# Performance work log

Hardware: AMD Instinct MI355X
Metric: run time of the kernel (lower is better)

The kernel has to match this reference:

```python
import jax, jax.numpy as jnp
import numpy as np

B, L, P = 64, 256, 32
LANE_DIM, EMBED, DEPTH, HEADS = 2, 128, 4, 8
MLP = 4 * EMBED
HD = EMBED // HEADS
MASK_RATIO, ELIG = 0.5, 5


def _glorot(key, shape):
    lim = float(np.sqrt(6.0 / (shape[-2] + shape[-1])))
    return jax.random.uniform(key, shape, jnp.float32, -lim, lim)


def setup_inputs() -> dict:
    key = jax.random.key(0)
    ks = jax.random.split(key, 24)
    lane_positions = jax.random.normal(ks[0], (B, L, P, LANE_DIM), jnp.float32)
    lane_centers = jax.random.normal(ks[1], (B, L, LANE_DIM), jnp.float32)
    lane_angles = jax.random.normal(ks[2], (B, L), jnp.float32)
    # ragged padding + random masking, precomputed (externalizes torch randperm loop)
    rng = np.random.default_rng(0)
    pad = rng.random((B, L, P)) < 0.2  # True = padding
    valid = ~pad
    num_valid = valid.sum(-1)                      # (B,L)
    eligible = num_valid > ELIG
    num_mask = (num_valid * MASK_RATIO).astype(np.int32)  # trunc == .int()
    scores = np.where(valid, rng.random((B, L, P)), 2.0)
    rank = scores.argsort(-1).argsort(-1)          # rank of each valid point
    sel = (rank < num_mask[..., None]) & valid & eligible[..., None]
    inp = {
        'lane_positions': lane_positions,
        'lane_centers': lane_centers,
        'lane_angles': lane_angles,
        'lane_padding_mask': jnp.asarray(pad),
        'sel_mask': jnp.asarray(sel),
        'Wp': _glorot(ks[3], (LANE_DIM, EMBED)), 'bp': jnp.zeros((EMBED,)),
        'Wpe1': _glorot(ks[4], (4, EMBED)), 'bpe1': jnp.zeros((EMBED,)),
        'Wpe2': _glorot(ks[5], (EMBED, EMBED)), 'bpe2': jnp.zeros((EMBED,)),
        'lane_type': 0.02 * jax.random.normal(ks[6], (EMBED,), jnp.float32),
        'mask_token': 0.02 * jax.random.normal(ks[7], (EMBED,), jnp.float32),
        'Wqkv': _glorot(ks[8], (DEPTH, EMBED, 3 * EMBED)), 'bqkv': jnp.zeros((DEPTH, 3 * EMBED)),
        'Wo': _glorot(ks[9], (DEPTH, EMBED, EMBED)), 'bo': jnp.zeros((DEPTH, EMBED)),
        'ln1_s': jnp.ones((DEPTH, EMBED)), 'ln1_b': jnp.zeros((DEPTH, EMBED)),
        'Wm1': _glorot(ks[10], (DEPTH, EMBED, MLP)), 'bm1': jnp.zeros((DEPTH, MLP)),
        'Wm2': _glorot(ks[11], (DEPTH, MLP, EMBED)), 'bm2': jnp.zeros((DEPTH, EMBED)),
        'ln2_s': jnp.ones((DEPTH, EMBED)), 'ln2_b': jnp.zeros((DEPTH, EMBED)),
        'lnf_s': jnp.ones((EMBED,)), 'lnf_b': jnp.zeros((EMBED,)),
        'Wd1': _glorot(ks[12], (EMBED, MLP)), 'bd1': jnp.zeros((MLP,)),
        'Wd2': _glorot(ks[13], (MLP, LANE_DIM)), 'bd2': jnp.zeros((LANE_DIM,)),
    }
    return inp


def _ln(x, s, b):
    m = jnp.mean(x, -1, keepdims=True)
    v = jnp.var(x, -1, keepdims=True)
    return (x - m) * jax.lax.rsqrt(v + 1e-5) * s + b


def _forward(lane_positions, lane_centers, lane_angles, Wp, bp, Wpe1, bpe1,
             Wpe2, bpe2, lane_type, mask_token, Wqkv, bqkv, Wo, bo, ln1_s,
             ln1_b, Wm1, bm1, Wm2, bm2, ln2_s, ln2_b, lnf_s, lnf_b, Wd1, bd1,
             Wd2, bd2, sel_mask):
    lane_norm = lane_positions - lane_centers[:, :, None, :]      # (B,L,P,2)
    feat = lane_norm @ Wp + bp                                    # (B,L,P,E)
    pos_feat = jnp.concatenate([lane_centers,
                                jnp.cos(lane_angles)[..., None],
                                jnp.sin(lane_angles)[..., None]], -1)  # (B,L,4)
    pe = jax.nn.gelu(pos_feat @ Wpe1 + bpe1, approximate=False) @ Wpe2 + bpe2
    tok = feat + pe[:, :, None, :] + lane_type
    tok = jnp.where(sel_mask[..., None], mask_token, tok)
    x = tok.reshape(B * L, P, EMBED)
    scale = 1.0 / np.sqrt(HD).astype(np.float32)
    for i in range(DEPTH):  # SpaNet: pre-LN transformer encoder over points
        h = _ln(x, ln1_s[i], ln1_b[i])
        q, k, v = jnp.split(h @ Wqkv[i] + bqkv[i], 3, axis=-1)
        q = q.reshape(B * L, P, HEADS, HD)
        k = k.reshape(B * L, P, HEADS, HD)
        v = v.reshape(B * L, P, HEADS, HD)
        att = jax.nn.softmax(jnp.einsum('nqhd,nkhd->nhqk', q, k) * scale, -1)
        o = jnp.einsum('nhqk,nkhd->nqhd', att, v).reshape(B * L, P, EMBED)
        x = x + o @ Wo[i] + bo[i]
        h = _ln(x, ln2_s[i], ln2_b[i])
        x = x + jax.nn.gelu(h @ Wm1[i] + bm1[i], approximate=False) @ Wm2[i] + bm2[i]
    x = _ln(x, lnf_s, lnf_b)
    y = (jax.nn.relu(x @ Wd1 + bd1) @ Wd2 + bd2).reshape(B, L, P, LANE_DIM)
    selc = sel_mask[..., None].astype(y.dtype)
    sq = (y - lane_norm) ** 2
    loss = jnp.sum(sq * selc) / jnp.maximum(jnp.sum(selc) * LANE_DIM, 1.0)
    return loss, y


def reference(lane_positions, lane_centers, lane_angles, lane_padding_mask,
              sel_mask, Wp, bp, Wpe1, bpe1, Wpe2, bpe2, lane_type, mask_token,
              Wqkv, bqkv, Wo, bo, ln1_s, ln1_b, Wm1, bm1, Wm2, bm2, ln2_s,
              ln2_b, lnf_s, lnf_b, Wd1, bd1, Wd2, bd2):
    del lane_padding_mask  # already folded into sel_mask during setup
    return _forward(lane_positions, lane_centers, lane_angles, Wp, bp, Wpe1,
                    bpe1, Wpe2, bpe2, lane_type, mask_token, Wqkv, bqkv, Wo,
                    bo, ln1_s, ln1_b, Wm1, bm1, Wm2, bm2, ln2_s, ln2_b, lnf_s,
                    lnf_b, Wd1, bd1, Wd2, bd2, sel_mask)
```

## Files before the change

kernel.cpp:

```cpp
#include <hip/hip_runtime.h>


#define NP 32
#define NE 128
#define NSEQ (64 * 256)
#define NMLP 512
#define NDEPTH 4
#define LST 132
#define HBS 136
#define H1C 264
#define QS  24
#define PS  40
#define VST 40

#define QKV_W_OFF 0
#define O_W_OFF   196608
#define M1_W_OFF  262144
#define M2_W_OFF  524288
#define D1_W_OFF  786432
#define W_TOTAL   851968

typedef unsigned short u16;
typedef unsigned int u32;
typedef __attribute__((ext_vector_type(8))) short bf16x8;
typedef __attribute__((ext_vector_type(4))) float f32x4;
typedef __attribute__((ext_vector_type(16))) float f32x16;
#define MFMA16 __builtin_amdgcn_mfma_f32_16x16x32_bf16
#define MFMA32 __builtin_amdgcn_mfma_f32_32x32x16_bf16

__device__ __forceinline__ float b2f(u16 u) {
  union { u32 i; float f; } v; v.i = ((u32)u) << 16; return v.f;
}
__device__ __forceinline__ u16 f2b(float f) {
  union { float f; u32 i; } v; v.f = f;
  u32 x = v.i;
  x += 0x7fffu + ((x >> 16) & 1u);
  return (u16)(x >> 16);
}
__device__ __forceinline__ u32 pk2(float lo, float hi) {
  return (u32)f2b(lo) | ((u32)f2b(hi) << 16);
}

__device__ __forceinline__ float gelu_f(float x) {
  float u = x * x;
  float a2 = x * fmaf(u, 0.07135481627466029f, 1.5957691216057308f);
  float e = __expf(a2);
  float r = __builtin_amdgcn_rcpf(e + 1.0f);
  return fmaf(-x, r, x);
}

struct Args {
  const float *pos, *ctr, *ang;
  const int *sel;
  const float *Wp, *bp, *Wpe1, *bpe1, *Wpe2, *bpe2, *ltype, *mtok;
  const float *Wqkv, *bqkv, *Wo, *bo, *ln1s, *ln1b, *Wm1, *bm1, *Wm2, *bm2;
  const float *ln2s, *ln2b, *lnfs, *lnfb, *Wd1, *bd1, *Wd2, *bd2;
  float* out;
  float* wsf;
  int* wsi;
};

__global__ void pack_w(const float* __restrict__ src, u16* __restrict__ dst,
                       int K, int N, int L, int scaleN, float scale) {
  int id = blockIdx.x * 256 + threadIdx.x;
  int KT = K >> 5, NT = N >> 4;
  int total = L * NT * KT * 64;
  if (id >= total) return;
  int lane = id & 63;
  int rest = id >> 6;
  int kt = rest % KT;
  int rest2 = rest / KT;
  int nt = rest2 % NT;
  int l = rest2 / NT;
  int col = nt * 16 + (lane & 15);
  float sc = (col < scaleN) ? scale : 1.0f;
  const float* s = src + (size_t)l * K * N + (size_t)(kt * 32 + (lane >> 4) * 8) * N + col;
  u16 tmp[8];
#pragma unroll
  for (int j = 0; j < 8; ++j) tmp[j] = f2b(s[(size_t)j * N] * sc);
  ((uint4*)dst)[id] = *(const uint4*)tmp;
}

template <int NTW>
__device__ __forceinline__ void gemm_kt4_b(const u16* __restrict__ hA,
                                           const u16* __restrict__ B, int w,
                                           int lane, const float* __restrict__ bias,
                                           f32x4 (&acc)[NTW][2]) {
  int ar = lane & 15, ac = (lane >> 4) * 8;
  bf16x8 af[8];
#pragma unroll
  for (int kb = 0; kb < 4; ++kb) {
    af[kb]     = *(const bf16x8*)(hA + ar * HBS + kb * 32 + ac);
    af[kb + 4] = *(const bf16x8*)(hA + (ar + 16) * HBS + kb * 32 + ac);
  }
#pragma unroll
  for (int i = 0; i < NTW; ++i) {
    int nt = w + 4 * i;
    const u16* Bp = B + (size_t)nt * 2048 + lane * 8;
    float bb = bias[nt * 16 + ar];
    f32x4 bi = {bb, bb, bb, bb};
    acc[i][0] = bi; acc[i][1] = bi;
#pragma unroll
    for (int kb = 0; kb < 4; ++kb) {
      bf16x8 b = *(const bf16x8*)(Bp + kb * 512);
      acc[i][0] = MFMA16(af[kb], b, acc[i][0], 0, 0, 0);
      acc[i][1] = MFMA16(af[kb + 4], b, acc[i][1], 0, 0, 0);
    }
  }
}

__device__ __forceinline__ void gemm_kt8_acc(const u16* __restrict__ hA,
                                             const u16* __restrict__ B, int ktoff,
                                             int w, int lane, f32x4 (&acc)[2][2]) {
  int ar = lane & 15, ac = (lane >> 4) * 8;
#pragma unroll
  for (int ktl = 0; ktl < 8; ++ktl) {
    bf16x8 a0 = *(const bf16x8*)(hA + ar * H1C + ktl * 32 + ac);
    bf16x8 a1 = *(const bf16x8*)(hA + (ar + 16) * H1C + ktl * 32 + ac);
#pragma unroll
    for (int i = 0; i < 2; ++i) {
      int nt = w + 4 * i;
      bf16x8 b = *(const bf16x8*)(B + (size_t)nt * 8192 + (size_t)(ktoff + ktl) * 512 + lane * 8);
      acc[i][0] = MFMA16(a0, b, acc[i][0], 0, 0, 0);
      acc[i][1] = MFMA16(a1, b, acc[i][1], 0, 0, 0);
    }
  }
}

__device__ __forceinline__ void layer_norm_bf(const float* __restrict__ src,
                                              u16* __restrict__ dst,
                                              const float* gam, const float* bet,
                                              int t, float* mrow, float* vrow) {
  int p = t >> 3, j0 = (t & 7) * 16;
  const float* row = src + p * LST + j0;
  float sum = 0.f, sq = 0.f;
#pragma unroll
  for (int k = 0; k < 16; ++k) { float v = row[k]; sum += v; sq += v * v; }
#pragma unroll
  for (int o = 1; o < 8; o <<= 1) { sum += __shfl_xor(sum, o); sq += __shfl_xor(sq, o); }
  if ((t & 7) == 0) {
    float m = sum * 0.0078125f;
    mrow[p] = m;
    vrow[p] = sq * 0.0078125f - m * m;
  }
  __syncthreads();
  float m = mrow[p], rs = rsqrtf(vrow[p] + 1e-5f);
  u32 wb[8];
#pragma unroll
  for (int k8 = 0; k8 < 4; ++k8) {
    float4 v = ((const float4*)row)[k8];
    float4 g = ((const float4*)(gam + j0))[k8];
    float4 b = ((const float4*)(bet + j0))[k8];
    wb[k8 * 2]     = pk2(fmaf((v.x - m) * rs, g.x, b.x), fmaf((v.y - m) * rs, g.y, b.y));
    wb[k8 * 2 + 1] = pk2(fmaf((v.z - m) * rs, g.z, b.z), fmaf((v.w - m) * rs, g.w, b.w));
  }
  uint4* dp = (uint4*)(dst + p * HBS + j0);
  dp[0] = make_uint4(wb[0], wb[1], wb[2], wb[3]);
  dp[1] = make_uint4(wb[4], wb[5], wb[6], wb[7]);
  __syncthreads();
}

__global__ __launch_bounds__(256, 3) void mrm_main_mfma(Args a, const u16* __restrict__ wsW) {
  __shared__ float xs[32 * LST];
  __shared__ __align__(16) u16 hbf[32 * HBS];
  __shared__ __align__(16) u16 uniu[10496];
  __shared__ float mrow[32], vrow[32];
  __shared__ int selv[32];
  __shared__ float lacc;

  u16* h1c = uniu;
  float* wd2s = (float*)(uniu + 8448);
  float* tvec = (float*)uniu;
  float* pvec = (float*)uniu + 128;

  const int s = blockIdx.x;
  const int t = threadIdx.x;
  const int w = t >> 6, lane = t & 63;
  const int cr = lane & 15, rq = (lane >> 4) * 4;
  const int rg = t >> 5, cg = t & 31, r0 = rg * 4, c0 = cg * 4;
  const int l15 = lane & 15, gl = lane >> 4;
  const int l31 = lane & 31, hi5 = lane >> 5;

  if (t == 0) lacc = 0.f;
  if (t < 32) selv[t] = a.sel[s * NP + t];

  const float cx = a.ctr[s * 2 + 0];
  const float cy = a.ctr[s * 2 + 1];
  const float an = a.ang[s];
  const float ca = __cosf(an), sa = __sinf(an);

  if (t < 128) {
    float accp = a.bpe1[t] + cx * a.Wpe1[t] + cy * a.Wpe1[128 + t]
               + ca * a.Wpe1[256 + t] + sa * a.Wpe1[384 + t];
    tvec[t] = gelu_f(accp);
  }
  __syncthreads();
  if (t < 128) {
    float accp = a.bpe2[t];
    for (int e = 0; e < 128; ++e) accp += tvec[e] * a.Wpe2[e * 128 + t];
    pvec[t] = accp;
  }
  __syncthreads();

  {
    float4 w0v = *(const float4*)(a.Wp + c0);
    float4 w1v = *(const float4*)(a.Wp + NE + c0);
    float4 bpv = *(const float4*)(a.bp + c0);
    float4 ltv = *(const float4*)(a.ltype + c0);
    float4 mtv = *(const float4*)(a.mtok + c0);
    float a0 = bpv.x + pvec[c0 + 0] + ltv.x;
    float a1 = bpv.y + pvec[c0 + 1] + ltv.y;
    float a2 = bpv.z + pvec[c0 + 2] + ltv.z;
    float a3 = bpv.w + pvec[c0 + 3] + ltv.w;
#pragma unroll
    for (int rr = 0; rr < 4; ++rr) {
      int p = r0 + rr;
      float px = a.pos[(s * NP + p) * 2 + 0] - cx;
      float py = a.pos[(s * NP + p) * 2 + 1] - cy;
      bool mk = selv[p] != 0;
      float4 o;
      o.x = mk ? mtv.x : (px * w0v.x + py * w1v.x + a0);
      o.y = mk ? mtv.y : (px * w0v.y + py * w1v.y + a1);
      o.z = mk ? mtv.z : (px * w0v.z + py * w1v.z + a2);
      o.w = mk ? mtv.w : (px * w0v.w + py * w1v.w + a3);
      *(float4*)&xs[p * LST + c0] = o;
    }
  }
  __syncthreads();

  u16* qb2 = uniu + w * 768;
  u16* kb2 = uniu + 3072 + w * 768;
  u16* vb2 = uniu + 6144 + w * 640;

  for (int li = 0; li < NDEPTH; ++li) {
    const u16* qkvW = wsW + QKV_W_OFF + li * 49152;
    const u16* oW   = wsW + O_W_OFF   + li * 16384;
    const u16* m1W  = wsW + M1_W_OFF  + li * 65536;
    const u16* m2W  = wsW + M2_W_OFF  + li * 65536;
    const float* bqkv_i = a.bqkv + li * 384;
    const float* bo_i   = a.bo + li * NE;
    const float* bm1_i  = a.bm1 + li * NMLP;
    const float* bm2_i  = a.bm2 + li * NE;

    layer_norm_bf(xs, hbf, a.ln1s + li * NE, a.ln1b + li * NE, t, mrow, vrow);

    u32 opk[2][2][2];
#pragma unroll
    for (int p = 0; p < 2; ++p) {
      const int hh = 4 * p + w;
      f32x4 acc[3][2];
      {
        int ar = lane & 15, ac = (lane >> 4) * 8;
        bf16x8 af[8];
#pragma unroll
        for (int kb = 0; kb < 4; ++kb) {
          af[kb]     = *(const bf16x8*)(hbf + ar * HBS + kb * 32 + ac);
          af[kb + 4] = *(const bf16x8*)(hbf + (ar + 16) * HBS + kb * 32 + ac);
        }
#pragma unroll
        for (int i = 0; i < 3; ++i) {
          int nt = i * 8 + hh;
          const u16* Bp = qkvW + (size_t)nt * 2048 + lane * 8;
          float bb = bqkv_i[nt * 16 + ar];
          if (i == 0) bb *= 0.25f;
          f32x4 bi = {bb, bb, bb, bb};
          acc[i][0] = bi; acc[i][1] = bi;
#pragma unroll
          for (int kb = 0; kb < 4; ++kb) {
            bf16x8 b = *(const bf16x8*)(Bp + kb * 512);
            acc[i][0] = MFMA16(af[kb], b, acc[i][0], 0, 0, 0);
            acc[i][1] = MFMA16(af[kb + 4], b, acc[i][1], 0, 0, 0);
          }
        }
      }
      {
#pragma unroll
        for (int j = 0; j < 4; ++j) {
          qb2[(rq + j) * QS + cr]      = f2b(acc[0][0][j]);
          qb2[(rq + j + 16) * QS + cr] = f2b(acc[0][1][j]);
          kb2[(rq + j) * QS + cr]      = f2b(acc[1][0][j]);
          kb2[(rq + j + 16) * QS + cr] = f2b(acc[1][1][j]);
        }
        u32* vbw = (u32*)vb2 + cr * 20 + (rq >> 1);
        vbw[0] = pk2(acc[2][0][0], acc[2][0][1]);
        vbw[1] = pk2(acc[2][0][2], acc[2][0][3]);
        vbw[8] = pk2(acc[2][1][0], acc[2][1][1]);
        vbw[9] = pk2(acc[2][1][2], acc[2][1][3]);
      }
      {
        bf16x8 kf = *(const bf16x8*)(kb2 + l31 * QS + hi5 * 8);
        bf16x8 qf = *(const bf16x8*)(qb2 + l31 * QS + hi5 * 8);
        f32x16 z16 = {0.f,0.f,0.f,0.f,0.f,0.f,0.f,0.f,0.f,0.f,0.f,0.f,0.f,0.f,0.f,0.f};
        f32x16 S = MFMA32(kf, qf, z16, 0, 0, 0);
        float mx = S[0];
#pragma unroll
        for (int r = 1; r < 16; ++r) mx = fmaxf(mx, S[r]);
        mx = fmaxf(mx, __shfl_xor(mx, 32));
        float sum = 0.f;
#pragma unroll
        for (int r = 0; r < 16; ++r) { S[r] = __expf(S[r] - mx); sum += S[r]; }
        sum += __shfl_xor(sum, 32);
        float inv = __builtin_amdgcn_rcpf(sum);
        u16* pb = ((l31 < 16) ? qb2 : kb2) + (l31 & 15) * PS;
#pragma unroll
        for (int i2 = 0; i2 < 8; ++i2) {
          int key0 = ((2 * i2) & 3) + 8 * (i2 >> 1) + 4 * hi5;
          *(u32*)(pb + key0) = pk2(S[2 * i2] * inv, S[2 * i2 + 1] * inv);
        }
        bf16x8 vf = *(const bf16x8*)(vb2 + l15 * VST + gl * 8);
        const f32x4 z = {0.f, 0.f, 0.f, 0.f};
#pragma unroll
        for (int qt = 0; qt < 2; ++qt) {
          bf16x8 pa = *(const bf16x8*)(((qt == 0) ? qb2 : kb2) + l15 * PS + gl * 8);
          f32x4 o = MFMA16(pa, vf, z, 0, 0, 0);
          opk[p][qt][0] = pk2(o[0], o[1]);
          opk[p][qt][1] = pk2(o[2], o[3]);
        }
      }
    }
    __syncthreads();
#pragma unroll
    for (int p = 0; p < 2; ++p) {
      const int hh = 4 * p + w;
#pragma unroll
      for (int qt = 0; qt < 2; ++qt) {
        u16* dst = hbf + (qt * 16 + gl * 4) * HBS + hh * 16 + l15;
        dst[0 * HBS] = (u16)opk[p][qt][0];
        dst[1 * HBS] = (u16)(opk[p][qt][0] >> 16);
        dst[2 * HBS] = (u16)opk[p][qt][1];
        dst[3 * HBS] = (u16)(opk[p][qt][1] >> 16);
      }
    }
    __syncthreads();

    {
      f32x4 acc[2][2];
      gemm_kt4_b<2>(hbf, oW, w, lane, bo_i, acc);
#pragma unroll
      for (int i = 0; i < 2; ++i) {
        int n = (w + 4 * i) * 16 + cr;
#pragma unroll
        for (int j = 0; j < 4; ++j) {
          xs[(rq + j) * LST + n]      += acc[i][0][j];
          xs[(rq + j + 16) * LST + n] += acc[i][1][j];
        }
      }
    }
    __syncthreads();

    layer_norm_bf(xs, hbf, a.ln2s + li * NE, a.ln2b + li * NE, t, mrow, vrow);

    {
      f32x4 acc2[2][2];
#pragma unroll
      for (int i = 0; i < 2; ++i) {
        float bb = bm2_i[(w + 4 * i) * 16 + cr];
        f32x4 bi = {bb, bb, bb, bb};
        acc2[i][0] = bi; acc2[i][1] = bi;
      }
#pragma unroll
      for (int ch = 0; ch < 2; ++ch) {
        {
          f32x4 acc[4][2];
          gemm_kt4_b<4>(hbf, m1W + ch * 32768, w, lane, bm1_i + ch * 256, acc);
#pragma unroll
          for (int i = 0; i < 4; ++i) {
            int nl = (w + 4 * i) * 16 + cr;
#pragma unroll
            for (int j = 0; j < 4; ++j) {
              h1c[(rq + j) * H1C + nl]      = f2b(gelu_f(acc[i][0][j]));
              h1c[(rq + j + 16) * H1C + nl] = f2b(gelu_f(acc[i][1][j]));
            }
          }
        }
        __syncthreads();
        gemm_kt8_acc(h1c, m2W, ch * 8, w, lane, acc2);
        __syncthreads();
      }
#pragma unroll
      for (int i = 0; i < 2; ++i) {
        int n = (w + 4 * i) * 16 + cr;
#pragma unroll
        for (int j = 0; j < 4; ++j) {
          xs[(rq + j) * LST + n]      += acc2[i][0][j];
          xs[(rq + j + 16) * LST + n] += acc2[i][1][j];
        }
      }
    }
    __syncthreads();
  }

  layer_norm_bf(xs, hbf, a.lnfs, a.lnfb, t, mrow, vrow);

  for (int i = t; i < 1024; i += 256) wd2s[i] = a.Wd2[i];

  float yacc = 0.f;
  const int pdec = t >> 3, dd2 = (t >> 2) & 1, q4 = t & 3;
#pragma unroll
  for (int ch = 0; ch < 2; ++ch) {
    {
      f32x4 acc[4][2];
      gemm_kt4_b<4>(hbf, wsW + D1_W_OFF + ch * 32768, w, lane, a.bd1 + ch * 256, acc);
#pragma unroll
      for (int i = 0; i < 4; ++i) {
        int nl = (w + 4 * i) * 16 + cr;
#pragma unroll
        for (int j = 0; j < 4; ++j) {
          h1c[(rq + j) * H1C + nl]      = f2b(fmaxf(acc[i][0][j], 0.f));
          h1c[(rq + j + 16) * H1C + nl] = f2b(fmaxf(acc[i][1][j], 0.f));
        }
      }
    }
    __syncthreads();
    {
      const u16* hrow = h1c + pdec * H1C + q4 * 64;
      const float* wp = wd2s + (ch * 256 + q4 * 64) * 2 + dd2;
#pragma unroll
      for (int k8 = 0; k8 < 8; ++k8) {
        bf16x8 hv = *(const bf16x8*)(hrow + k8 * 8);
#pragma unroll
        for (int jj = 0; jj < 8; ++jj)
          yacc += b2f((u16)hv[jj]) * wp[(k8 * 8 + jj) * 2];
      }
    }
    __syncthreads();
  }

  {
    yacc += __shfl_xor(yacc, 1);
    yacc += __shfl_xor(yacc, 2);
    if (q4 == 0) {
      float y = yacc + a.bd2[dd2];
      a.out[1 + (s * NP + pdec) * 2 + dd2] = y;
      float lnm = a.pos[(s * NP + pdec) * 2 + dd2] - (dd2 ? cy : cx);
      float d = y - lnm;
      if (selv[pdec] != 0) atomicAdd(&lacc, d * d);
    }
  }
  __syncthreads();
  if (t == 0) {
    atomicAdd(a.wsf, lacc);
    int cnt = 0;
#pragma unroll
    for (int p = 0; p < NP; ++p) cnt += (selv[p] != 0) ? 1 : 0;
    atomicAdd(a.wsi, cnt);
  }
}

__global__ void mrm_fin(const float* ws, float* out) {
  float num = ws[0];
  int cnt = ((const int*)ws)[1];
  float den = fmaxf((float)cnt * 2.0f, 1.0f);
  out[0] = num / den;
}

extern "C" void kernel_launch(void* const* d_in, const int* in_sizes, int n_in,
                              void* d_out, int out_size, void* d_ws, size_t ws_size,
                              hipStream_t stream) {
  (void)in_sizes; (void)n_in; (void)out_size; (void)ws_size;
  Args a;
  a.pos   = (const float*)d_in[0];
  a.ctr   = (const float*)d_in[1];
  a.ang   = (const float*)d_in[2];
  a.sel   = (const int*)d_in[4];
  a.Wp    = (const float*)d_in[5];
  a.bp    = (const float*)d_in[6];
  a.Wpe1  = (const float*)d_in[7];
  a.bpe1  = (const float*)d_in[8];
  a.Wpe2  = (const float*)d_in[9];
  a.bpe2  = (const float*)d_in[10];
  a.ltype = (const float*)d_in[11];
  a.mtok  = (const float*)d_in[12];
  a.Wqkv  = (const float*)d_in[13];
  a.bqkv  = (const float*)d_in[14];
  a.Wo    = (const float*)d_in[15];
  a.bo    = (const float*)d_in[16];
  a.ln1s  = (const float*)d_in[17];
  a.ln1b  = (const float*)d_in[18];
  a.Wm1   = (const float*)d_in[19];
  a.bm1   = (const float*)d_in[20];
  a.Wm2   = (const float*)d_in[21];
  a.bm2   = (const float*)d_in[22];
  a.ln2s  = (const float*)d_in[23];
  a.ln2b  = (const float*)d_in[24];
  a.lnfs  = (const float*)d_in[25];
  a.lnfb  = (const float*)d_in[26];
  a.Wd1   = (const float*)d_in[27];
  a.bd1   = (const float*)d_in[28];
  a.Wd2   = (const float*)d_in[29];
  a.bd2   = (const float*)d_in[30];
  a.out   = (float*)d_out;
  a.wsf   = (float*)d_ws;
  a.wsi   = ((int*)d_ws) + 1;

  hipMemsetAsync(d_ws, 0, 8, stream);
  u16* wsW = (u16*)((char*)d_ws + 64);
  pack_w<<<dim3(96),  dim3(256), 0, stream>>>(a.Wqkv, wsW + QKV_W_OFF, 128, 384, 4, 128, 0.25f);
  pack_w<<<dim3(32),  dim3(256), 0, stream>>>(a.Wo,   wsW + O_W_OFF,   128, 128, 4, 0, 1.f);
  pack_w<<<dim3(128), dim3(256), 0, stream>>>(a.Wm1,  wsW + M1_W_OFF,  128, 512, 4, 0, 1.f);
  pack_w<<<dim3(128), dim3(256), 0, stream>>>(a.Wm2,  wsW + M2_W_OFF,  512, 128, 4, 0, 1.f);
  pack_w<<<dim3(32),  dim3(256), 0, stream>>>(a.Wd1,  wsW + D1_W_OFF,  128, 512, 1, 0, 1.f);
  mrm_main_mfma<<<dim3(NSEQ), dim3(256), 0, stream>>>(a, wsW);
  mrm_fin<<<dim3(1), dim3(1), 0, stream>>>((const float*)d_ws, (float*)d_out);
}
```

Measured before the change: 2.131 ms.

## Keep residual stream in registers, shrink LDS, raise occupancy to four blocks

The fp32 residual tile moves from shared memory into per-thread registers laid out to match the MFMA output fragments. Layer norm becomes a register-based macro that reduces partial sums through a small shared buffer. The Wd2 shared copy is dropped, its reads now come from global memory, and positions are staged once in shared memory. With the smaller LDS footprint, launch bounds rise from three to four blocks per CU. Other changes: bf16 conversion now uses the library intrinsic, and the softmax max/sum use tree reductions. The risks are higher register pressure under the tighter bound and an extra barrier in each layer norm.

```diff
diff --git a/kernel.cpp b/kernel.cpp
--- a/kernel.cpp
+++ b/kernel.cpp
@@ -1,4 +1,5 @@
 #include <hip/hip_runtime.h>
+#include <hip/hip_bf16.h>
 
 
 #define NP 32
@@ -6,12 +7,12 @@
 #define NSEQ (64 * 256)
 #define NMLP 512
 #define NDEPTH 4
-#define LST 132
 #define HBS 136
 #define H1C 264
 #define QS  24
 #define PS  40
 #define VST 40
+#define PBS 66
 
 #define QKV_W_OFF 0
 #define O_W_OFF   196608
@@ -32,10 +33,8 @@
   union { u32 i; float f; } v; v.i = ((u32)u) << 16; return v.f;
 }
 __device__ __forceinline__ u16 f2b(float f) {
-  union { float f; u32 i; } v; v.f = f;
-  u32 x = v.i;
-  x += 0x7fffu + ((x >> 16) & 1u);
-  return (u16)(x >> 16);
+  __hip_bfloat16 h = __float2bfloat16(f);
+  union { __hip_bfloat16 h; u16 u; } v; v.h = h; return v.u;
 }
 __device__ __forceinline__ u32 pk2(float lo, float hi) {
   return (u32)f2b(lo) | ((u32)f2b(hi) << 16);
@@ -127,49 +126,17 @@
   }
 }
 
-__device__ __forceinline__ void layer_norm_bf(const float* __restrict__ src,
-                                              u16* __restrict__ dst,
-                                              const float* gam, const float* bet,
-                                              int t, float* mrow, float* vrow) {
-  int p = t >> 3, j0 = (t & 7) * 16;
-  const float* row = src + p * LST + j0;
-  float sum = 0.f, sq = 0.f;
-#pragma unroll
-  for (int k = 0; k < 16; ++k) { float v = row[k]; sum += v; sq += v * v; }
-#pragma unroll
-  for (int o = 1; o < 8; o <<= 1) { sum += __shfl_xor(sum, o); sq += __shfl_xor(sq, o); }
-  if ((t & 7) == 0) {
-    float m = sum * 0.0078125f;
-    mrow[p] = m;
-    vrow[p] = sq * 0.0078125f - m * m;
-  }
-  __syncthreads();
-  float m = mrow[p], rs = rsqrtf(vrow[p] + 1e-5f);
-  u32 wb[8];
-#pragma unroll
-  for (int k8 = 0; k8 < 4; ++k8) {
-    float4 v = ((const float4*)row)[k8];
-    float4 g = ((const float4*)(gam + j0))[k8];
-    float4 b = ((const float4*)(bet + j0))[k8];
-    wb[k8 * 2]     = pk2(fmaf((v.x - m) * rs, g.x, b.x), fmaf((v.y - m) * rs, g.y, b.y));
-    wb[k8 * 2 + 1] = pk2(fmaf((v.z - m) * rs, g.z, b.z), fmaf((v.w - m) * rs, g.w, b.w));
-  }
-  uint4* dp = (uint4*)(dst + p * HBS + j0);
-  dp[0] = make_uint4(wb[0], wb[1], wb[2], wb[3]);
-  dp[1] = make_uint4(wb[4], wb[5], wb[6], wb[7]);
-  __syncthreads();
-}
-
-__global__ __launch_bounds__(256, 3) void mrm_main_mfma(Args a, const u16* __restrict__ wsW) {
-  __shared__ float xs[32 * LST];
+__global__ __launch_bounds__(256, 4) void mrm_main_mfma(Args a, const u16* __restrict__ wsW) {
   __shared__ __align__(16) u16 hbf[32 * HBS];
-  __shared__ __align__(16) u16 uniu[10496];
+  __shared__ __align__(16) u16 uniu[8704];
+  __shared__ float posb[64];
   __shared__ float mrow[32], vrow[32];
   __shared__ int selv[32];
   __shared__ float lacc;
 
   u16* h1c = uniu;
-  float* wd2s = (float*)(uniu + 8448);
+  float* pbufS = (float*)uniu;
+  float* pbufQ = (float*)(uniu + 4224);
   float* tvec = (float*)uniu;
   float* pvec = (float*)uniu + 128;
 
@@ -177,12 +144,12 @@
   const int t = threadIdx.x;
   const int w = t >> 6, lane = t & 63;
   const int cr = lane & 15, rq = (lane >> 4) * 4;
-  const int rg = t >> 5, cg = t & 31, r0 = rg * 4, c0 = cg * 4;
   const int l15 = lane & 15, gl = lane >> 4;
   const int l31 = lane & 31, hi5 = lane >> 5;
 
   if (t == 0) lacc = 0.f;
   if (t < 32) selv[t] = a.sel[s * NP + t];
+  if (t < 64) posb[t] = a.pos[s * 64 + t];
 
   const float cx = a.ctr[s * 2 + 0];
   const float cy = a.ctr[s * 2 + 1];
@@ -202,35 +169,89 @@
   }
   __syncthreads();
 
+  float xr[16];
   {
-    float4 w0v = *(const float4*)(a.Wp + c0);
-    float4 w1v = *(const float4*)(a.Wp + NE + c0);
-    float4 bpv = *(const float4*)(a.bp + c0);
-    float4 ltv = *(const float4*)(a.ltype + c0);
-    float4 mtv = *(const float4*)(a.mtok + c0);
-    float a0 = bpv.x + pvec[c0 + 0] + ltv.x;
-    float a1 = bpv.y + pvec[c0 + 1] + ltv.y;
-    float a2 = bpv.z + pvec[c0 + 2] + ltv.z;
-    float a3 = bpv.w + pvec[c0 + 3] + ltv.w;
-#pragma unroll
-    for (int rr = 0; rr < 4; ++rr) {
-      int p = r0 + rr;
-      float px = a.pos[(s * NP + p) * 2 + 0] - cx;
-      float py = a.pos[(s * NP + p) * 2 + 1] - cy;
-      bool mk = selv[p] != 0;
-      float4 o;
-      o.x = mk ? mtv.x : (px * w0v.x + py * w1v.x + a0);
-      o.y = mk ? mtv.y : (px * w0v.y + py * w1v.y + a1);
-      o.z = mk ? mtv.z : (px * w0v.z + py * w1v.z + a2);
-      o.w = mk ? mtv.w : (px * w0v.w + py * w1v.w + a3);
-      *(float4*)&xs[p * LST + c0] = o;
-    }
+    float wpn[2], wpn2[2], addc[2], mtv[2];
+#pragma unroll
+    for (int i = 0; i < 2; ++i) {
+      int n = (w + 4 * i) * 16 + cr;
+      wpn[i] = a.Wp[n];
+      wpn2[i] = a.Wp[128 + n];
+      addc[i] = a.bp[n] + pvec[n] + a.ltype[n];
+      mtv[i] = a.mtok[n];
+    }
+#pragma unroll
+    for (int h = 0; h < 2; ++h)
+#pragma unroll
+      for (int j = 0; j < 4; ++j) {
+        int p = rq + j + 16 * h;
+        float px = posb[p * 2 + 0] - cx;
+        float py = posb[p * 2 + 1] - cy;
+        bool mk = selv[p] != 0;
+#pragma unroll
+        for (int i = 0; i < 2; ++i)
+          xr[h * 8 + i * 4 + j] = mk ? mtv[i] : fmaf(px, wpn[i], fmaf(py, wpn2[i], addc[i]));
+      }
   }
   __syncthreads();
 
   u16* qb2 = uniu + w * 768;
   u16* kb2 = uniu + 3072 + w * 768;
   u16* vb2 = uniu + 6144 + w * 640;
+
+#define LN_REG(GAM, BET)                                                       \
+  {                                                                            \
+    _Pragma("unroll")                                                          \
+    for (int h = 0; h < 2; ++h)                                                \
+      _Pragma("unroll")                                                        \
+      for (int j = 0; j < 4; ++j) {                                            \
+        float x0 = xr[h * 8 + j], x1 = xr[h * 8 + 4 + j];                      \
+        int row = rq + j + 16 * h;                                             \
+        pbufS[row * PBS + w * 16 + cr] = x0 + x1;                              \
+        pbufQ[row * PBS + w * 16 + cr] = x0 * x0 + x1 * x1;                    \
+      }                                                                        \
+    __syncthreads();                                                           \
+    {                                                                          \
+      int p = t >> 3, j8 = t & 7;                                              \
+      const float* bs = pbufS + p * PBS + j8 * 8;                              \
+      const float* bq = pbufQ + p * PBS + j8 * 8;                              \
+      float sum = 0.f, sq = 0.f;                                               \
+      _Pragma("unroll")                                                        \
+      for (int k = 0; k < 8; ++k) { sum += bs[k]; sq += bq[k]; }               \
+      _Pragma("unroll")                                                        \
+      for (int o = 1; o < 8; o <<= 1) {                                        \
+        sum += __shfl_xor(sum, o); sq += __shfl_xor(sq, o);                    \
+      }                                                                        \
+      if (j8 == 0) {                                                           \
+        float m = sum * 0.0078125f;                                            \
+        mrow[p] = m;                                                           \
+        vrow[p] = sq * 0.0078125f - m * m;                                     \
+      }                                                                        \
+    }                                                                          \
+    __syncthreads();                                                           \
+    {                                                                          \
+      float gv[2], bv[2];                                                      \
+      _Pragma("unroll")                                                        \
+      for (int i = 0; i < 2; ++i) {                                            \
+        int n = (w + 4 * i) * 16 + cr;                                         \
+        gv[i] = (GAM)[n]; bv[i] = (BET)[n];                                    \
+      }                                                                        \
+      _Pragma("unroll")                                                        \
+      for (int h = 0; h < 2; ++h)                                              \
+        _Pragma("unroll")                                                      \
+        for (int j = 0; j < 4; ++j) {                                          \
+          int row = rq + j + 16 * h;                                           \
+          float m = mrow[row], rs = rsqrtf(vrow[row] + 1e-5f);                 \
+          _Pragma("unroll")                                                    \
+          for (int i = 0; i < 2; ++i) {                                        \
+            int n = (w + 4 * i) * 16 + cr;                                     \
+            float hv = fmaf((xr[h * 8 + i * 4 + j] - m) * rs, gv[i], bv[i]);   \
+            hbf[row * HBS + n] = f2b(hv);                                      \
+          }                                                                    \
+        }                                                                      \
+    }                                                                          \
+    __syncthreads();                                                           \
+  }
 
   for (int li = 0; li < NDEPTH; ++li) {
     const u16* qkvW = wsW + QKV_W_OFF + li * 49152;
@@ -242,7 +263,7 @@
     const float* bm1_i  = a.bm1 + li * NMLP;
     const float* bm2_i  = a.bm2 + li * NE;
 
-    layer_norm_bf(xs, hbf, a.ln1s + li * NE, a.ln1b + li * NE, t, mrow, vrow);
+    LN_REG(a.ln1s + li * NE, a.ln1b + li * NE);
 
     u32 opk[2][2][2];
 #pragma unroll
@@ -292,13 +313,17 @@
         bf16x8 qf = *(const bf16x8*)(qb2 + l31 * QS + hi5 * 8);
         f32x16 z16 = {0.f,0.f,0.f,0.f,0.f,0.f,0.f,0.f,0.f,0.f,0.f,0.f,0.f,0.f,0.f,0.f};
         f32x16 S = MFMA32(kf, qf, z16, 0, 0, 0);
-        float mx = S[0];
-#pragma unroll
-        for (int r = 1; r < 16; ++r) mx = fmaxf(mx, S[r]);
+        float m01 = fmaxf(S[0], S[1]),   m23 = fmaxf(S[2], S[3]);
+        float m45 = fmaxf(S[4], S[5]),   m67 = fmaxf(S[6], S[7]);
+        float m89 = fmaxf(S[8], S[9]),   mab = fmaxf(S[10], S[11]);
+        float mcd = fmaxf(S[12], S[13]), mef = fmaxf(S[14], S[15]);
+        float mx = fmaxf(fmaxf(fmaxf(m01, m23), fmaxf(m45, m67)),
+                         fmaxf(fmaxf(m89, mab), fmaxf(mcd, mef)));
         mx = fmaxf(mx, __shfl_xor(mx, 32));
-        float sum = 0.f;
-#pragma unroll
-        for (int r = 0; r < 16; ++r) { S[r] = __expf(S[r] - mx); sum += S[r]; }
+#pragma unroll
+        for (int r = 0; r < 16; ++r) S[r] = __expf(S[r] - mx);
+        float sum = ((S[0] + S[1]) + (S[2] + S[3])) + ((S[4] + S[5]) + (S[6] + S[7]))
+                  + ((S[8] + S[9]) + (S[10] + S[11])) + ((S[12] + S[13]) + (S[14] + S[15]));
         sum += __shfl_xor(sum, 32);
         float inv = __builtin_amdgcn_rcpf(sum);
         u16* pb = ((l31 < 16) ? qb2 : kb2) + (l31 & 15) * PS;
@@ -337,18 +362,15 @@
       f32x4 acc[2][2];
       gemm_kt4_b<2>(hbf, oW, w, lane, bo_i, acc);
 #pragma unroll
-      for (int i = 0; i < 2; ++i) {
-        int n = (w + 4 * i) * 16 + cr;
+      for (int i = 0; i < 2; ++i)
 #pragma unroll
         for (int j = 0; j < 4; ++j) {
-          xs[(rq + j) * LST + n]      += acc[i][0][j];
-          xs[(rq + j + 16) * LST + n] += acc[i][1][j];
-        }
-      }
-    }
-    __syncthreads();
-
-    layer_norm_bf(xs, hbf, a.ln2s + li * NE, a.ln2b + li * NE, t, mrow, vrow);
+          xr[0 + i * 4 + j] += acc[i][0][j];
+          xr[8 + i * 4 + j] += acc[i][1][j];
+        }
+    }
+
+    LN_REG(a.ln2s + li * NE, a.ln2b + li * NE);
 
     {
       f32x4 acc2[2][2];
@@ -378,21 +400,16 @@
         __syncthreads();
       }
 #pragma unroll
-      for (int i = 0; i < 2; ++i) {
-        int n = (w + 4 * i) * 16 + cr;
+      for (int i = 0; i < 2; ++i)
 #pragma unroll
         for (int j = 0; j < 4; ++j) {
-          xs[(rq + j) * LST + n]      += acc2[i][0][j];
-          xs[(rq + j + 16) * LST + n] += acc2[i][1][j];
-        }
-      }
-    }
-    __syncthreads();
-  }
-
-  layer_norm_bf(xs, hbf, a.lnfs, a.lnfb, t, mrow, vrow);
-
-  for (int i = t; i < 1024; i += 256) wd2s[i] = a.Wd2[i];
+          xr[0 + i * 4 + j] += acc2[i][0][j];
+          xr[8 + i * 4 + j] += acc2[i][1][j];
+        }
+    }
+  }
+
+  LN_REG(a.lnfs, a.lnfb);
 
   float yacc = 0.f;
   const int pdec = t >> 3, dd2 = (t >> 2) & 1, q4 = t & 3;
@@ -414,7 +431,7 @@
     __syncthreads();
     {
       const u16* hrow = h1c + pdec * H1C + q4 * 64;
-      const float* wp = wd2s + (ch * 256 + q4 * 64) * 2 + dd2;
+      const float* wp = a.Wd2 + (ch * 256 + q4 * 64) * 2 + dd2;
 #pragma unroll
       for (int k8 = 0; k8 < 8; ++k8) {
         bf16x8 hv = *(const bf16x8*)(hrow + k8 * 8);
@@ -432,7 +449,7 @@
     if (q4 == 0) {
       float y = yacc + a.bd2[dd2];
       a.out[1 + (s * NP + pdec) * 2 + dd2] = y;
-      float lnm = a.pos[(s * NP + pdec) * 2 + dd2] - (dd2 ? cy : cx);
+      float lnm = posb[pdec * 2 + dd2] - (dd2 ? cy : cx);
       float d = y - lnm;
       if (selv[pdec] != 0) atomicAdd(&lacc, d * d);
     }
```

Result: slower. 3.265 ms (+53.2%).
